# Kernel optimization log

Hardware: AMD Instinct MI355X
Metric: run time of the kernel (lower is better)

## Reference

```python
import jax, jax.numpy as jnp
import numpy as np

EPS = 1e-6
HEAD_DIM = 128
NUM_HEADS = 16
NUM_KV_HEADS = 8
HIDDEN = 2048
BATCH = 32
NUM_BLOCKS = 4096
BLOCK_SIZE = 16
MAX_BLOCKS = 128


def rmsnorm(x, w):
    # x: [..., head_dim]; per-head RMSNorm as in Qwen3
    var = jnp.mean(jnp.square(x), axis=-1, keepdims=True)
    return x * jax.lax.rsqrt(var + EPS) * w


def apply_rope(x, cos, sin):
    # x: [B, H, D]; cos/sin: [B, D] broadcast over heads
    d2 = x.shape[-1] // 2
    x1, x2 = x[..., :d2], x[..., d2:]
    rot = jnp.concatenate([-x2, x1], axis=-1)
    return x * cos[:, None, :] + rot * sin[:, None, :]


def setup_inputs() -> dict:
    key = jax.random.key(0)
    ks = jax.random.split(key, 13)
    s = 0.02
    hidden_states = jax.random.normal(ks[0], (BATCH, HIDDEN), dtype=jnp.float32)
    cos = jax.random.uniform(ks[1], (BATCH, HEAD_DIM), minval=-1.0, maxval=1.0, dtype=jnp.float32)
    sin = jax.random.uniform(ks[2], (BATCH, HEAD_DIM), minval=-1.0, maxval=1.0, dtype=jnp.float32)
    k_cache = jax.random.normal(ks[3], (NUM_BLOCKS, BLOCK_SIZE, NUM_KV_HEADS, HEAD_DIM), dtype=jnp.float32)
    v_cache = jax.random.normal(ks[4], (NUM_BLOCKS, BLOCK_SIZE, NUM_KV_HEADS, HEAD_DIM), dtype=jnp.float32)
    block_tables = jax.random.randint(ks[5], (BATCH, MAX_BLOCKS), 0, NUM_BLOCKS, dtype=jnp.int32)
    context_lens = jax.random.randint(ks[6], (BATCH,), 1, MAX_BLOCKS * BLOCK_SIZE + 1, dtype=jnp.int32)
    wq = jax.random.normal(ks[7], (HIDDEN, NUM_HEADS * HEAD_DIM), dtype=jnp.float32) * s
    wk = jax.random.normal(ks[8], (HIDDEN, NUM_KV_HEADS * HEAD_DIM), dtype=jnp.float32) * s
    wv = jax.random.normal(ks[9], (HIDDEN, NUM_KV_HEADS * HEAD_DIM), dtype=jnp.float32) * s
    wo = jax.random.normal(ks[10], (NUM_HEADS * HEAD_DIM, HIDDEN), dtype=jnp.float32) * s
    q_norm_w = jnp.ones((HEAD_DIM,), dtype=jnp.float32) + 0.1 * jax.random.normal(ks[11], (HEAD_DIM,), dtype=jnp.float32)
    k_norm_w = jnp.ones((HEAD_DIM,), dtype=jnp.float32) + 0.1 * jax.random.normal(ks[12], (HEAD_DIM,), dtype=jnp.float32)
    return dict(hidden_states=hidden_states, cos=cos, sin=sin, k_cache=k_cache, v_cache=v_cache,
                wq=wq, wk=wk, wv=wv, wo=wo, q_norm_w=q_norm_w, k_norm_w=k_norm_w,
                block_tables=block_tables, context_lens=context_lens)


def reference(hidden_states, cos, sin, k_cache, v_cache, wq, wk, wv, wo,
              q_norm_w, k_norm_w, block_tables, context_lens):
    B = hidden_states.shape[0]
    D = q_norm_w.shape[0]
    H = wq.shape[1] // D
    KVH = wk.shape[1] // D
    n_rep = H // KVH
    block_size = k_cache.shape[1]
    max_blocks = block_tables.shape[1]
    L = max_blocks * block_size  # max padded context length
    scale = 1.0 / np.sqrt(D).astype(np.float32)

    # QKV projections (decode: one token per sequence)
    q = (hidden_states @ wq).reshape(B, H, D)
    k = (hidden_states @ wk).reshape(B, KVH, D)
    v = (hidden_states @ wv).reshape(B, KVH, D)

    # Per-head RMSNorm then RoPE (Qwen3 ordering)
    q = apply_rope(rmsnorm(q, q_norm_w), cos, sin)
    k = apply_rope(rmsnorm(k, k_norm_w), cos, sin)

    # Paged gather of KV blocks: [B, max_blocks, block_size, KVH, D] -> [B, L, KVH, D]
    valid_blocks = jnp.clip(block_tables, 0, None)
    kg = k_cache[valid_blocks].reshape(B, L, KVH, D)
    vg = v_cache[valid_blocks].reshape(B, L, KVH, D)

    # GQA attention without materializing repeated K/V: group q as [B, KVH, n_rep, D]
    qg = q.reshape(B, KVH, n_rep, D)
    scores = jnp.einsum('bgrd,blgd->bgrl', qg, kg) * scale  # [B, KVH, n_rep, L]
    mask = jnp.arange(L, dtype=jnp.int32)[None, :] >= context_lens[:, None]  # [B, L]
    scores = jnp.where(mask[:, None, None, :], -jnp.inf, scores)
    attn = jax.nn.softmax(scores, axis=-1)
    out = jnp.einsum('bgrl,blgd->bgrd', attn, vg).reshape(B, H * D)
    output = out @ wo  # [B, hidden]
    return output, k, v
```

## Files before the change

### kernel.cpp

```cpp
#include <hip/hip_runtime.h>

#define HIDDEN 2048
#define HEAD_DIM 128
#define NUM_KV 8
#define BATCH 32
#define MAX_PAGES 128
#define PAGE 16
#define QKV_COLS 4096
#define KSPLIT1 16
#define KCH1 (HIDDEN / KSPLIT1)
#define CSPLIT 8
#define PAGES_PER_SPLIT (MAX_PAGES / CSPLIT)
#define KSPLIT2 16
#define KCH2 (HIDDEN / KSPLIT2)

#define WS_QKVP 0
#define WS_QBUF 2097152
#define WS_AOUT 2162688
#define WS_PACC 0
#define WS_PML  524288
#define WS_OUTP 0

__global__ __launch_bounds__(128) void qkv_partial_kernel(
    const float* __restrict__ x, const float* __restrict__ wq,
    const float* __restrict__ wk, const float* __restrict__ wv,
    float* __restrict__ part) {
  int n = blockIdx.x * 128 + threadIdx.x;
  int kz = blockIdx.y;
  int k0 = kz * KCH1;
  const float* W; int ldw, col;
  if (n < 2048)      { W = wq; ldw = 2048; col = n; }
  else if (n < 3072) { W = wk; ldw = 1024; col = n - 2048; }
  else               { W = wv; ldw = 1024; col = n - 3072; }
  float acc[BATCH];
#pragma unroll
  for (int b = 0; b < BATCH; ++b) acc[b] = 0.f;
#pragma unroll 4
  for (int kk = 0; kk < KCH1; ++kk) {
    int k = k0 + kk;
    float w = W[(size_t)k * ldw + col];
#pragma unroll
    for (int b = 0; b < BATCH; ++b)
      acc[b] = fmaf(x[b * HIDDEN + k], w, acc[b]);
  }
#pragma unroll
  for (int b = 0; b < BATCH; ++b)
    part[((size_t)kz * BATCH + b) * QKV_COLS + n] = acc[b];
}

__global__ __launch_bounds__(128) void qkv_finish_kernel(
    const float* __restrict__ part, const float* __restrict__ cosb,
    const float* __restrict__ sinb, const float* __restrict__ qnw,
    const float* __restrict__ knw, float* __restrict__ qbuf,
    float* __restrict__ outk, float* __restrict__ outv) {
  int b = blockIdx.x;
  int s = blockIdx.y;
  int d = threadIdx.x;
  int col;
  if (s < 16)      col = s * 128 + d;
  else if (s < 24) col = 2048 + (s - 16) * 128 + d;
  else             col = 3072 + (s - 24) * 128 + d;
  float val = 0.f;
#pragma unroll
  for (int z = 0; z < KSPLIT1; ++z)
    val += part[((size_t)z * BATCH + b) * QKV_COLS + col];
  if (s >= 24) {
    outv[b * 1024 + (s - 24) * 128 + d] = val;
    return;
  }
  __shared__ float red[128];
  __shared__ float xs[128];
  red[d] = val * val;
  __syncthreads();
#pragma unroll
  for (int st = 64; st > 0; st >>= 1) {
    if (d < st) red[d] += red[d + st];
    __syncthreads();
  }
  float var = red[0] * (1.f / 128.f);
  float inv = rsqrtf(var + 1e-6f);
  const float* nw = (s < 16) ? qnw : knw;
  float xn = val * inv * nw[d];
  xs[d] = xn;
  __syncthreads();
  float c  = cosb[b * 128 + d];
  float sn = sinb[b * 128 + d];
  float rot = (d < 64) ? -xs[d + 64] : xs[d - 64];
  float o = xn * c + rot * sn;
  if (s < 16) qbuf[b * 2048 + s * 128 + d] = o;
  else        outk[b * 1024 + (s - 16) * 128 + d] = o;
}

__global__ __launch_bounds__(256) void attn_kernel(
    const float* __restrict__ qbuf, const float* __restrict__ kc,
    const float* __restrict__ vc, const int* __restrict__ btab,
    const int* __restrict__ clen, float* __restrict__ pacc,
    float* __restrict__ pml) {
  int b = blockIdx.x, g = blockIdx.y, sp = blockIdx.z;
  int tid = threadIdx.x;
  __shared__ float v_s[PAGE][HEAD_DIM];
  __shared__ float s_s[2][PAGE];
  const float NEG_INF = -__builtin_huge_valf();
  int ctx = clen[b];
  int npages = (ctx + PAGE - 1) >> 4;
  int p0 = sp * PAGES_PER_SPLIT;
  int p1 = min(p0 + PAGES_PER_SPLIT, npages);

  int pos = tid >> 4, dp = tid & 15;
  float ql0[8], ql1[8];
  {
    const float4* q0 = (const float4*)(qbuf + b * 2048 + (g * 2 + 0) * 128 + dp * 8);
    const float4* q1 = (const float4*)(qbuf + b * 2048 + (g * 2 + 1) * 128 + dp * 8);
    float4 a = q0[0], c = q0[1];
    ql0[0]=a.x; ql0[1]=a.y; ql0[2]=a.z; ql0[3]=a.w;
    ql0[4]=c.x; ql0[5]=c.y; ql0[6]=c.z; ql0[7]=c.w;
    a = q1[0]; c = q1[1];
    ql1[0]=a.x; ql1[1]=a.y; ql1[2]=a.z; ql1[3]=a.w;
    ql1[4]=c.x; ql1[5]=c.y; ql1[6]=c.z; ql1[7]=c.w;
  }
  int r2 = tid >> 7, d2 = tid & 127;
  float acc = 0.f, lsum = 0.f, m = NEG_INF;
  const float scale = 0.08838834764831845f;

  for (int p = p0; p < p1; ++p) {
    int page = btab[b * MAX_PAGES + p];
    size_t base = ((size_t)(page * PAGE + pos) * NUM_KV + g) * HEAD_DIM + dp * 8;
    const float4* kp = (const float4*)(kc + base);
    const float4* vp = (const float4*)(vc + base);
    float4 k0 = kp[0], k1 = kp[1];
    float4 v0 = vp[0], v1 = vp[1];
    float s0 = 0.f, s1 = 0.f;
    s0 = fmaf(k0.x, ql0[0], s0); s1 = fmaf(k0.x, ql1[0], s1);
    s0 = fmaf(k0.y, ql0[1], s0); s1 = fmaf(k0.y, ql1[1], s1);
    s0 = fmaf(k0.z, ql0[2], s0); s1 = fmaf(k0.z, ql1[2], s1);
    s0 = fmaf(k0.w, ql0[3], s0); s1 = fmaf(k0.w, ql1[3], s1);
    s0 = fmaf(k1.x, ql0[4], s0); s1 = fmaf(k1.x, ql1[4], s1);
    s0 = fmaf(k1.y, ql0[5], s0); s1 = fmaf(k1.y, ql1[5], s1);
    s0 = fmaf(k1.z, ql0[6], s0); s1 = fmaf(k1.z, ql1[6], s1);
    s0 = fmaf(k1.w, ql0[7], s0); s1 = fmaf(k1.w, ql1[7], s1);
#pragma unroll
    for (int off = 1; off < 16; off <<= 1) {
      s0 += __shfl_xor(s0, off);
      s1 += __shfl_xor(s1, off);
    }
    *(float4*)(&v_s[pos][dp * 8])     = v0;
    *(float4*)(&v_s[pos][dp * 8 + 4]) = v1;
    if (dp == 0) {
      bool valid = (p * PAGE + pos) < ctx;
      s_s[0][pos] = valid ? s0 * scale : NEG_INF;
      s_s[1][pos] = valid ? s1 * scale : NEG_INF;
    }
    __syncthreads();
    const float* srow = s_s[r2];
    float cmax = NEG_INF;
#pragma unroll
    for (int l = 0; l < PAGE; ++l) cmax = fmaxf(cmax, srow[l]);
    float mnew = fmaxf(m, cmax);
    float alpha = __expf(m - mnew);
    acc *= alpha; lsum *= alpha;
#pragma unroll
    for (int l = 0; l < PAGE; ++l) {
      float w = __expf(srow[l] - mnew);
      lsum += w;
      acc = fmaf(w, v_s[l][d2], acc);
    }
    m = mnew;
    __syncthreads();
  }
  size_t pidx = ((size_t)b * NUM_KV + g) * CSPLIT + sp;
  pacc[pidx * 256 + tid] = acc;
  if (d2 == 0) {
    pml[pidx * 4 + r2 * 2 + 0] = m;
    pml[pidx * 4 + r2 * 2 + 1] = lsum;
  }
}

__global__ __launch_bounds__(256) void attn_combine_kernel(
    const float* __restrict__ pacc, const float* __restrict__ pml,
    float* __restrict__ attn_out) {
  int b = blockIdx.x, g = blockIdx.y, tid = threadIdx.x;
  int r = tid >> 7, d = tid & 127;
  size_t base = ((size_t)b * NUM_KV + g) * CSPLIT;
  float M = -__builtin_huge_valf();
#pragma unroll
  for (int s = 0; s < CSPLIT; ++s)
    M = fmaxf(M, pml[(base + s) * 4 + r * 2]);
  float accT = 0.f, lT = 0.f;
#pragma unroll
  for (int s = 0; s < CSPLIT; ++s) {
    float ms = pml[(base + s) * 4 + r * 2];
    float ls = pml[(base + s) * 4 + r * 2 + 1];
    float w = __expf(ms - M);
    accT = fmaf(w, pacc[(base + s) * 256 + tid], accT);
    lT = fmaf(w, ls, lT);
  }
  attn_out[b * 2048 + (g * 2 + r) * 128 + d] = accT / lT;
}

__global__ __launch_bounds__(128) void out_partial_kernel(
    const float* __restrict__ ain, const float* __restrict__ wo,
    float* __restrict__ part) {
  int n = blockIdx.x * 128 + threadIdx.x;
  int kz = blockIdx.y;
  int k0 = kz * KCH2;
  float acc[BATCH];
#pragma unroll
  for (int b = 0; b < BATCH; ++b) acc[b] = 0.f;
#pragma unroll 4
  for (int kk = 0; kk < KCH2; ++kk) {
    int k = k0 + kk;
    float w = wo[(size_t)k * HIDDEN + n];
#pragma unroll
    for (int b = 0; b < BATCH; ++b)
      acc[b] = fmaf(ain[b * HIDDEN + k], w, acc[b]);
  }
#pragma unroll
  for (int b = 0; b < BATCH; ++b)
    part[(size_t)kz * (BATCH * HIDDEN) + b * HIDDEN + n] = acc[b];
}

__global__ __launch_bounds__(256) void out_finish_kernel(
    const float* __restrict__ part, float* __restrict__ outp) {
  int idx = blockIdx.x * 256 + threadIdx.x;
  float v = 0.f;
#pragma unroll
  for (int z = 0; z < KSPLIT2; ++z)
    v += part[(size_t)z * (BATCH * HIDDEN) + idx];
  outp[idx] = v;
}

extern "C" void kernel_launch(void* const* d_in, const int* in_sizes, int n_in,
                              void* d_out, int out_size, void* d_ws, size_t ws_size,
                              hipStream_t stream) {
  const float* hidden = (const float*)d_in[0];
  const float* cosb   = (const float*)d_in[1];
  const float* sinb   = (const float*)d_in[2];
  const float* kc     = (const float*)d_in[3];
  const float* vc     = (const float*)d_in[4];
  const float* wq     = (const float*)d_in[5];
  const float* wk     = (const float*)d_in[6];
  const float* wv     = (const float*)d_in[7];
  const float* wo     = (const float*)d_in[8];
  const float* qnw    = (const float*)d_in[9];
  const float* knw    = (const float*)d_in[10];
  const int* btab     = (const int*)d_in[11];
  const int* clen     = (const int*)d_in[12];
  float* out = (float*)d_out;
  float* ws  = (float*)d_ws;

  float* qkvp = ws + WS_QKVP;
  float* qbuf = ws + WS_QBUF;
  float* aout = ws + WS_AOUT;
  float* pacc = ws + WS_PACC;
  float* pml  = ws + WS_PML;
  float* outp = ws + WS_OUTP;

  float* outO = out;
  float* outK = out + 65536;
  float* outV = out + 98304;

  hipLaunchKernelGGL(qkv_partial_kernel, dim3(32, KSPLIT1), dim3(128), 0, stream,
                     hidden, wq, wk, wv, qkvp);
  hipLaunchKernelGGL(qkv_finish_kernel, dim3(32, 32), dim3(128), 0, stream,
                     qkvp, cosb, sinb, qnw, knw, qbuf, outK, outV);
  hipLaunchKernelGGL(attn_kernel, dim3(BATCH, NUM_KV, CSPLIT), dim3(256), 0, stream,
                     qbuf, kc, vc, btab, clen, pacc, pml);
  hipLaunchKernelGGL(attn_combine_kernel, dim3(BATCH, NUM_KV), dim3(256), 0, stream,
                     pacc, pml, aout);
  hipLaunchKernelGGL(out_partial_kernel, dim3(16, KSPLIT2), dim3(128), 0, stream,
                     aout, wo, outp);
  hipLaunchKernelGGL(out_finish_kernel, dim3(256), dim3(256), 0, stream,
                     outp, outO);
}
```

Measured before the change: 617.3 us.

## Double-buffer weight loads, raise K-splits, and prefetch KV pages with per-lane online softmax

The two GEMV-style kernels now use a K-split of 32 instead of 16 and software-pipeline their weight loads in two 8-element register buffers, so loads overlap the FMAs. The attention kernel drops the per-page shared-memory staging and both barriers. Each lane group instead keeps its own online softmax and prefetches the next page's K/V into registers, and the 16 per-position partials are merged through shared memory once at the end. This targets memory latency and synchronisation cost, at the price of more registers, larger partial buffers and more reduction traffic in the finish kernels.

Result: faster. 589.9 us (-4.4%).

```diff
diff --git a/kernel.cpp b/kernel.cpp
--- a/kernel.cpp
+++ b/kernel.cpp
@@ -7,16 +7,16 @@
 #define MAX_PAGES 128
 #define PAGE 16
 #define QKV_COLS 4096
-#define KSPLIT1 16
+#define KSPLIT1 32
 #define KCH1 (HIDDEN / KSPLIT1)
 #define CSPLIT 8
 #define PAGES_PER_SPLIT (MAX_PAGES / CSPLIT)
-#define KSPLIT2 16
+#define KSPLIT2 32
 #define KCH2 (HIDDEN / KSPLIT2)
 
 #define WS_QKVP 0
-#define WS_QBUF 2097152
-#define WS_AOUT 2162688
+#define WS_QBUF 4194304
+#define WS_AOUT 4259840
 #define WS_PACC 0
 #define WS_PML  524288
 #define WS_OUTP 0
@@ -32,16 +32,33 @@
   if (n < 2048)      { W = wq; ldw = 2048; col = n; }
   else if (n < 3072) { W = wk; ldw = 1024; col = n - 2048; }
   else               { W = wv; ldw = 1024; col = n - 3072; }
+  const float* Wp = W + (size_t)k0 * ldw + col;
   float acc[BATCH];
 #pragma unroll
   for (int b = 0; b < BATCH; ++b) acc[b] = 0.f;
-#pragma unroll 4
-  for (int kk = 0; kk < KCH1; ++kk) {
-    int k = k0 + kk;
-    float w = W[(size_t)k * ldw + col];
-#pragma unroll
-    for (int b = 0; b < BATCH; ++b)
-      acc[b] = fmaf(x[b * HIDDEN + k], w, acc[b]);
+  float wa[8], wb[8];
+#pragma unroll
+  for (int j = 0; j < 8; ++j) wa[j] = Wp[(size_t)j * ldw];
+#pragma unroll
+  for (int kk = 0; kk < KCH1; kk += 16) {
+#pragma unroll
+    for (int j = 0; j < 8; ++j) wb[j] = Wp[(size_t)(kk + 8 + j) * ldw];
+#pragma unroll
+    for (int j = 0; j < 8; ++j) {
+#pragma unroll
+      for (int b = 0; b < BATCH; ++b)
+        acc[b] = fmaf(x[b * HIDDEN + k0 + kk + j], wa[j], acc[b]);
+    }
+    if (kk + 16 < KCH1) {
+#pragma unroll
+      for (int j = 0; j < 8; ++j) wa[j] = Wp[(size_t)(kk + 16 + j) * ldw];
+    }
+#pragma unroll
+    for (int j = 0; j < 8; ++j) {
+#pragma unroll
+      for (int b = 0; b < BATCH; ++b)
+        acc[b] = fmaf(x[b * HIDDEN + k0 + kk + 8 + j], wb[j], acc[b]);
+    }
   }
 #pragma unroll
   for (int b = 0; b < BATCH; ++b)
@@ -98,8 +115,6 @@
     float* __restrict__ pml) {
   int b = blockIdx.x, g = blockIdx.y, sp = blockIdx.z;
   int tid = threadIdx.x;
-  __shared__ float v_s[PAGE][HEAD_DIM];
-  __shared__ float s_s[2][PAGE];
   const float NEG_INF = -__builtin_huge_valf();
   int ctx = clen[b];
   int npages = (ctx + PAGE - 1) >> 4;
@@ -118,60 +133,105 @@
     ql1[0]=a.x; ql1[1]=a.y; ql1[2]=a.z; ql1[3]=a.w;
     ql1[4]=c.x; ql1[5]=c.y; ql1[6]=c.z; ql1[7]=c.w;
   }
-  int r2 = tid >> 7, d2 = tid & 127;
-  float acc = 0.f, lsum = 0.f, m = NEG_INF;
+  float acc0[8], acc1[8];
+#pragma unroll
+  for (int j = 0; j < 8; ++j) { acc0[j] = 0.f; acc1[j] = 0.f; }
+  float m0 = NEG_INF, m1 = NEG_INF, l0 = 0.f, l1 = 0.f;
   const float scale = 0.08838834764831845f;
 
-  for (int p = p0; p < p1; ++p) {
-    int page = btab[b * MAX_PAGES + p];
+  float4 ck0, ck1, cv0, cv1;
+  if (p0 < p1) {
+    int page = btab[b * MAX_PAGES + p0];
     size_t base = ((size_t)(page * PAGE + pos) * NUM_KV + g) * HEAD_DIM + dp * 8;
     const float4* kp = (const float4*)(kc + base);
     const float4* vp = (const float4*)(vc + base);
-    float4 k0 = kp[0], k1 = kp[1];
-    float4 v0 = vp[0], v1 = vp[1];
+    ck0 = kp[0]; ck1 = kp[1]; cv0 = vp[0]; cv1 = vp[1];
+  }
+  for (int p = p0; p < p1; ++p) {
+    float4 nk0, nk1, nv0, nv1;
+    if (p + 1 < p1) {
+      int page = btab[b * MAX_PAGES + p + 1];
+      size_t base = ((size_t)(page * PAGE + pos) * NUM_KV + g) * HEAD_DIM + dp * 8;
+      const float4* kp = (const float4*)(kc + base);
+      const float4* vp = (const float4*)(vc + base);
+      nk0 = kp[0]; nk1 = kp[1]; nv0 = vp[0]; nv1 = vp[1];
+    }
     float s0 = 0.f, s1 = 0.f;
-    s0 = fmaf(k0.x, ql0[0], s0); s1 = fmaf(k0.x, ql1[0], s1);
-    s0 = fmaf(k0.y, ql0[1], s0); s1 = fmaf(k0.y, ql1[1], s1);
-    s0 = fmaf(k0.z, ql0[2], s0); s1 = fmaf(k0.z, ql1[2], s1);
-    s0 = fmaf(k0.w, ql0[3], s0); s1 = fmaf(k0.w, ql1[3], s1);
-    s0 = fmaf(k1.x, ql0[4], s0); s1 = fmaf(k1.x, ql1[4], s1);
-    s0 = fmaf(k1.y, ql0[5], s0); s1 = fmaf(k1.y, ql1[5], s1);
-    s0 = fmaf(k1.z, ql0[6], s0); s1 = fmaf(k1.z, ql1[6], s1);
-    s0 = fmaf(k1.w, ql0[7], s0); s1 = fmaf(k1.w, ql1[7], s1);
+    s0 = fmaf(ck0.x, ql0[0], s0); s1 = fmaf(ck0.x, ql1[0], s1);
+    s0 = fmaf(ck0.y, ql0[1], s0); s1 = fmaf(ck0.y, ql1[1], s1);
+    s0 = fmaf(ck0.z, ql0[2], s0); s1 = fmaf(ck0.z, ql1[2], s1);
+    s0 = fmaf(ck0.w, ql0[3], s0); s1 = fmaf(ck0.w, ql1[3], s1);
+    s0 = fmaf(ck1.x, ql0[4], s0); s1 = fmaf(ck1.x, ql1[4], s1);
+    s0 = fmaf(ck1.y, ql0[5], s0); s1 = fmaf(ck1.y, ql1[5], s1);
+    s0 = fmaf(ck1.z, ql0[6], s0); s1 = fmaf(ck1.z, ql1[6], s1);
+    s0 = fmaf(ck1.w, ql0[7], s0); s1 = fmaf(ck1.w, ql1[7], s1);
 #pragma unroll
     for (int off = 1; off < 16; off <<= 1) {
       s0 += __shfl_xor(s0, off);
       s1 += __shfl_xor(s1, off);
     }
-    *(float4*)(&v_s[pos][dp * 8])     = v0;
-    *(float4*)(&v_s[pos][dp * 8 + 4]) = v1;
-    if (dp == 0) {
-      bool valid = (p * PAGE + pos) < ctx;
-      s_s[0][pos] = valid ? s0 * scale : NEG_INF;
-      s_s[1][pos] = valid ? s1 * scale : NEG_INF;
-    }
-    __syncthreads();
-    const float* srow = s_s[r2];
-    float cmax = NEG_INF;
-#pragma unroll
-    for (int l = 0; l < PAGE; ++l) cmax = fmaxf(cmax, srow[l]);
-    float mnew = fmaxf(m, cmax);
-    float alpha = __expf(m - mnew);
-    acc *= alpha; lsum *= alpha;
-#pragma unroll
-    for (int l = 0; l < PAGE; ++l) {
-      float w = __expf(srow[l] - mnew);
-      lsum += w;
-      acc = fmaf(w, v_s[l][d2], acc);
-    }
-    m = mnew;
-    __syncthreads();
+    bool valid = (p * PAGE + pos) < ctx;
+    if (valid) {
+      float t0 = s0 * scale;
+      float mn = fmaxf(m0, t0);
+      float a  = __expf(m0 - mn);
+      float w  = __expf(t0 - mn);
+      l0 = fmaf(l0, a, w); m0 = mn;
+      acc0[0] = fmaf(acc0[0], a, w * cv0.x);
+      acc0[1] = fmaf(acc0[1], a, w * cv0.y);
+      acc0[2] = fmaf(acc0[2], a, w * cv0.z);
+      acc0[3] = fmaf(acc0[3], a, w * cv0.w);
+      acc0[4] = fmaf(acc0[4], a, w * cv1.x);
+      acc0[5] = fmaf(acc0[5], a, w * cv1.y);
+      acc0[6] = fmaf(acc0[6], a, w * cv1.z);
+      acc0[7] = fmaf(acc0[7], a, w * cv1.w);
+      float t1 = s1 * scale;
+      float mn1 = fmaxf(m1, t1);
+      float a1  = __expf(m1 - mn1);
+      float w1  = __expf(t1 - mn1);
+      l1 = fmaf(l1, a1, w1); m1 = mn1;
+      acc1[0] = fmaf(acc1[0], a1, w1 * cv0.x);
+      acc1[1] = fmaf(acc1[1], a1, w1 * cv0.y);
+      acc1[2] = fmaf(acc1[2], a1, w1 * cv0.z);
+      acc1[3] = fmaf(acc1[3], a1, w1 * cv0.w);
+      acc1[4] = fmaf(acc1[4], a1, w1 * cv1.x);
+      acc1[5] = fmaf(acc1[5], a1, w1 * cv1.y);
+      acc1[6] = fmaf(acc1[6], a1, w1 * cv1.z);
+      acc1[7] = fmaf(acc1[7], a1, w1 * cv1.w);
+    }
+    ck0 = nk0; ck1 = nk1; cv0 = nv0; cv1 = nv1;
+  }
+
+  __shared__ float m_s[2][16], l_s[2][16];
+  __shared__ float acc_s[2][16][128];
+  if (dp == 0) {
+    m_s[0][pos] = m0; m_s[1][pos] = m1;
+    l_s[0][pos] = l0; l_s[1][pos] = l1;
+  }
+#pragma unroll
+  for (int j = 0; j < 8; ++j) {
+    acc_s[0][pos][dp * 8 + j] = acc0[j];
+    acc_s[1][pos][dp * 8 + j] = acc1[j];
+  }
+  __syncthreads();
+  int r2 = tid >> 7, d2 = tid & 127;
+  float M = NEG_INF;
+#pragma unroll
+  for (int q = 0; q < 16; ++q) M = fmaxf(M, m_s[r2][q]);
+  float accT = 0.f, lT = 0.f;
+  if (M != NEG_INF) {
+#pragma unroll
+    for (int q = 0; q < 16; ++q) {
+      float w = __expf(m_s[r2][q] - M);
+      accT = fmaf(w, acc_s[r2][q][d2], accT);
+      lT   = fmaf(w, l_s[r2][q], lT);
+    }
   }
   size_t pidx = ((size_t)b * NUM_KV + g) * CSPLIT + sp;
-  pacc[pidx * 256 + tid] = acc;
+  pacc[pidx * 256 + tid] = accT;
   if (d2 == 0) {
-    pml[pidx * 4 + r2 * 2 + 0] = m;
-    pml[pidx * 4 + r2 * 2 + 1] = lsum;
+    pml[pidx * 4 + r2 * 2 + 0] = M;
+    pml[pidx * 4 + r2 * 2 + 1] = lT;
   }
 }
 
@@ -203,16 +263,33 @@
   int n = blockIdx.x * 128 + threadIdx.x;
   int kz = blockIdx.y;
   int k0 = kz * KCH2;
+  const float* Wp = wo + (size_t)k0 * HIDDEN + n;
   float acc[BATCH];
 #pragma unroll
   for (int b = 0; b < BATCH; ++b) acc[b] = 0.f;
-#pragma unroll 4
-  for (int kk = 0; kk < KCH2; ++kk) {
-    int k = k0 + kk;
-    float w = wo[(size_t)k * HIDDEN + n];
-#pragma unroll
-    for (int b = 0; b < BATCH; ++b)
-      acc[b] = fmaf(ain[b * HIDDEN + k], w, acc[b]);
+  float wa[8], wb[8];
+#pragma unroll
+  for (int j = 0; j < 8; ++j) wa[j] = Wp[(size_t)j * HIDDEN];
+#pragma unroll
+  for (int kk = 0; kk < KCH2; kk += 16) {
+#pragma unroll
+    for (int j = 0; j < 8; ++j) wb[j] = Wp[(size_t)(kk + 8 + j) * HIDDEN];
+#pragma unroll
+    for (int j = 0; j < 8; ++j) {
+#pragma unroll
+      for (int b = 0; b < BATCH; ++b)
+        acc[b] = fmaf(ain[b * HIDDEN + k0 + kk + j], wa[j], acc[b]);
+    }
+    if (kk + 16 < KCH2) {
+#pragma unroll
+      for (int j = 0; j < 8; ++j) wa[j] = Wp[(size_t)(kk + 16 + j) * HIDDEN];
+    }
+#pragma unroll
+    for (int j = 0; j < 8; ++j) {
+#pragma unroll
+      for (int b = 0; b < BATCH; ++b)
+        acc[b] = fmaf(ain[b * HIDDEN + k0 + kk + 8 + j], wb[j], acc[b]);
+    }
   }
 #pragma unroll
   for (int b = 0; b < BATCH; ++b)
```
